# Kernel optimization log

Measured on AMD Instinct MI355X. Metric: run time of the kernel, lower is better.

## Reference

```python
import jax, jax.numpy as jnp
import numpy as np

N_NODES = 100000
N_EDGES = 1600000


def gcn_conv(x, row, col, norm, W, b, n_nodes):
    # PyG GCNConv: h = x @ W; aggregate normalized messages over (A + I); add bias
    h = x @ W                                   # [N, out]
    msg = h[col] * norm[:, None]                # [E+N, out] gather + scale
    out = jax.ops.segment_sum(msg, row, num_segments=n_nodes)  # scatter-add
    return out + b


def _norm_and_loops(edge_index, n_nodes):
    # add self-loops, compute symmetric normalization coefficients
    row = jnp.concatenate([edge_index[0], jnp.arange(n_nodes, dtype=edge_index.dtype)])
    col = jnp.concatenate([edge_index[1], jnp.arange(n_nodes, dtype=edge_index.dtype)])
    deg = jax.ops.segment_sum(jnp.ones_like(row, dtype=jnp.float32), row,
                              num_segments=n_nodes)
    dinv = jnp.where(deg > 0, jax.lax.rsqrt(deg), 0.0)
    norm = dinv[row] * dinv[col]
    return row, col, norm


def reference(x, edge_index, W1, b1, W2, b2, W3, b3):
    n_nodes = x.shape[0]
    row, col, norm = _norm_and_loops(edge_index, n_nodes)
    h = jax.nn.relu(gcn_conv(x, row, col, norm, W1, b1, n_nodes))
    h = jax.nn.relu(gcn_conv(h, row, col, norm, W2, b2, n_nodes))
    h = gcn_conv(h, row, col, norm, W3, b3, n_nodes)
    return jax.nn.log_softmax(h, axis=1)


def setup_inputs() -> dict:
    key = jax.random.key(0)
    ks = jax.random.split(key, 5)
    d_in, d_hid, d_out = 128, 128, 16
    x = jax.random.normal(ks[0], (N_NODES, d_in), dtype=jnp.float32)
    edge_index = jax.random.randint(ks[1], (2, N_EDGES), 0, N_NODES, dtype=jnp.int64)
    s1 = 1.0 / np.sqrt(d_in)
    s3 = 1.0 / np.sqrt(d_hid)
    W1 = jax.random.normal(ks[2], (d_in, d_hid), dtype=jnp.float32) * s1
    W2 = jax.random.normal(ks[3], (d_hid, d_hid), dtype=jnp.float32) * s3
    W3 = jax.random.normal(ks[4], (d_hid, d_out), dtype=jnp.float32) * s3
    return {
        "x": x, "edge_index": edge_index,
        "W1": W1, "b1": jnp.zeros((d_hid,), jnp.float32),
        "W2": W2, "b2": jnp.zeros((d_hid,), jnp.float32),
        "W3": W3, "b3": jnp.zeros((d_out,), jnp.float32),
    }
```

## Files before the change

kernel.cpp:

```cpp
#include <hip/hip_runtime.h>

typedef unsigned int u32;
typedef _Float16 f16;
typedef __attribute__((ext_vector_type(8))) _Float16 half8;
typedef __attribute__((ext_vector_type(2))) _Float16 half2_t;
typedef __attribute__((ext_vector_type(4))) float f32x4;

#define D_IN 128
#define D_HID 128
#define D_OUT 16
#define RPB 128
#define MAXBUCK 1024
#define CHUNK 16384
#define PGRAN 4
#define SLACK 2048


__global__ __launch_bounds__(256) void detect_k(const int* __restrict__ ei,
                                                u32* __restrict__ flag, int n) {
    int i = blockIdx.x * 256 + threadIdx.x;
    if (i < n && (i & 1) && ei[i] != 0) atomicOr(flag, 1u);
}

__device__ inline int load_row(const int* ei, u32 f, int e, int E) {
    return f ? ei[e] : ei[2 * e];
}
__device__ inline int load_col(const int* ei, u32 f, int e, int E) {
    return f ? ei[E + e] : ei[2 * E + 2 * e];
}
__device__ inline int clampi(int v, int n) {
    v = v < 0 ? 0 : v;
    return v >= n ? n - 1 : v;
}
__device__ inline u32 al16(u32 v) { return (v + 15u) & ~15u; }

__global__ __launch_bounds__(256) void hist_k(const int* __restrict__ ei,
                                              const u32* __restrict__ flag,
                                              u32* __restrict__ Hmat,
                                              int E, int N, int NBK, int NB) {
    __shared__ u32 lh[MAXBUCK];
    int tid = threadIdx.x;
    for (int i = tid; i < NBK; i += 256) lh[i] = 0;
    __syncthreads();
    u32 f = *flag;
    int base = blockIdx.x * CHUNK;
    int lim = base + CHUNK < E ? base + CHUNK : E;
    for (int e = base + tid; e < lim; e += 256) {
        int r = clampi(load_row(ei, f, e, E), N);
        atomicAdd(&lh[(u32)r >> 7], 1u);
    }
    __syncthreads();
    for (int i = tid; i < NBK; i += 256)
        Hmat[(size_t)i * NB + blockIdx.x] = lh[i];
}

__global__ __launch_bounds__(256) void scan1(const u32* __restrict__ cnt,
                                             u32* __restrict__ excl,
                                             u32* __restrict__ partial, int n) {
    __shared__ u32 sm[256];
    int tid = threadIdx.x;
    int i = blockIdx.x * 256 + tid;
    u32 v = (i < n) ? cnt[i] : 0u;
    sm[tid] = v;
    __syncthreads();
    for (int off = 1; off < 256; off <<= 1) {
        u32 t = (tid >= off) ? sm[tid - off] : 0u;
        __syncthreads();
        sm[tid] += t;
        __syncthreads();
    }
    if (i < n) excl[i] = sm[tid] - v;
    if (tid == 255) partial[blockIdx.x] = sm[255];
}

__global__ __launch_bounds__(512) void scan2(u32* __restrict__ partial, int nb) {
    __shared__ u32 sm[512];
    int tid = threadIdx.x;
    u32 v = (tid < nb) ? partial[tid] : 0u;
    sm[tid] = v;
    __syncthreads();
    for (int off = 1; off < 512; off <<= 1) {
        u32 t = (tid >= off) ? sm[tid - off] : 0u;
        __syncthreads();
        sm[tid] += t;
        __syncthreads();
    }
    if (tid < nb) partial[tid] = sm[tid] - v;
}

__global__ __launch_bounds__(256) void scan3(u32* __restrict__ excl,
                                             const u32* __restrict__ partial,
                                             int n, int E) {
    int i = blockIdx.x * 256 + threadIdx.x;
    if (i < n) excl[i] += partial[blockIdx.x];
    if (i == 0) excl[n] = (u32)E;
}

__global__ __launch_bounds__(256) void scatter_bd(const int* __restrict__ ei,
                                                  const u32* __restrict__ flag,
                                                  const u32* __restrict__ Hbase,
                                                  u32* __restrict__ bdata,
                                                  int E, int N, int NBK, int NB) {
    __shared__ u32 lbase[MAXBUCK];
    int tid = threadIdx.x;
    for (int i = tid; i < NBK; i += 256)
        lbase[i] = Hbase[(size_t)i * NB + blockIdx.x];
    __syncthreads();
    u32 f = *flag;
    int base = blockIdx.x * CHUNK;
    int lim = base + CHUNK < E ? base + CHUNK : E;
    for (int e = base + tid; e < lim; e += 256) {
        int r = clampi(load_row(ei, f, e, E), N);
        int c = clampi(load_col(ei, f, e, E), N);
        u32 pos = atomicAdd(&lbase[(u32)r >> 7], 1u);
        if (pos < (u32)E) bdata[pos] = ((u32)(r & (RPB - 1)) << 20) | (u32)c;
    }
}

__global__ __launch_bounds__(256) void finalize_k(const u32* __restrict__ bdata,
                                                  const u32* __restrict__ Hbase,
                                                  u32* __restrict__ row_start,
                                                  u32* __restrict__ rend,
                                                  float* __restrict__ dinv,
                                                  u32* __restrict__ ecol,
                                                  int N, int E, int NB) {
    __shared__ u32 smc[RPB];
    __shared__ u32 cur[RPB];
    int b = blockIdx.x;
    int tid = threadIdx.x;
    u32 s = Hbase[(size_t)b * NB];
    u32 t = Hbase[(size_t)(b + 1) * NB];
    u32 pbase = al16(s) + (u32)b * SLACK;
    if (tid < RPB) smc[tid] = 0;
    __syncthreads();
    for (u32 i = s + tid; i < t; i += 256)
        atomicAdd(&smc[bdata[i] >> 20], 1u);
    __syncthreads();
    u32 deg = (tid < RPB) ? smc[tid] : 0;
    u32 pdeg = (deg + PGRAN - 1) & ~(u32)(PGRAN - 1);
    if (tid < RPB) smc[tid] = pdeg;
    __syncthreads();
    for (int off = 1; off < RPB; off <<= 1) {
        u32 tv = (tid < RPB && tid >= off) ? smc[tid - off] : 0u;
        __syncthreads();
        if (tid < RPB) smc[tid] += tv;
        __syncthreads();
    }
    u32 pexcl = (tid < RPB) ? (smc[tid] - pdeg) : 0;
    if (tid < RPB) {
        int r = b * RPB + tid;
        if (r < N) {
            row_start[r] = pbase + pexcl;
            rend[r] = pbase + pexcl + pdeg;
            dinv[r] = rsqrtf((float)(deg + 1u));
        }
        cur[tid] = pbase + pexcl;
    }
    __syncthreads();
    for (u32 i = s + tid; i < t; i += 256) {
        u32 rec = bdata[i];
        u32 pos = atomicAdd(&cur[rec >> 20], 1u);
        ecol[pos] = rec & 0xFFFFFu;
    }
    __syncthreads();
    if (tid < RPB) {
        u32 st = pbase + pexcl;
        for (u32 k = deg; k < pdeg; k++) ecol[st + k] = (u32)N;
    }
}

__global__ __launch_bounds__(256) void reformat_all(const float* __restrict__ W1,
                                                    const float* __restrict__ W2,
                                                    const float* __restrict__ W3,
                                                    f16* __restrict__ W1h, f16* __restrict__ W1l,
                                                    f16* __restrict__ W2h, f16* __restrict__ W2l,
                                                    f16* __restrict__ W3h, f16* __restrict__ W3l,
                                                    f16* __restrict__ hzero,
                                                    f16* __restrict__ h3zero) {
    if (blockIdx.x == 17) {
        int tix = threadIdx.x;
        if (tix < 128) hzero[tix] = (f16)0;
        else if (tix < 144) h3zero[tix - 128] = (f16)0;
        return;
    }
    const float* W;
    f16 *Wh, *Wl;
    int ntiles, bidx;
    if (blockIdx.x < 8) { W = W1; Wh = W1h; Wl = W1l; ntiles = 8; bidx = blockIdx.x; }
    else if (blockIdx.x < 16) { W = W2; Wh = W2h; Wl = W2l; ntiles = 8; bidx = blockIdx.x - 8; }
    else { W = W3; Wh = W3h; Wl = W3l; ntiles = 1; bidx = 0; }
    int idx = bidx * 256 + threadIdx.x;
    int total = 4 * ntiles * 64;
    if (idx >= total) return;
    int lane = idx & 63;
    int st = idx >> 6;
    int t = st % ntiles;
    int s = st / ntiles;
    int Nc = ntiles * 16;
    int n = t * 16 + (lane & 15);
    int kb = lane >> 4;
    half8 vh, vl;
#pragma unroll
    for (int j = 0; j < 8; j++) {
        float w = W[(size_t)(s * 32 + kb * 8 + j) * Nc + n];
        f16 hi = (f16)w;
        f16 lo = (f16)(w - (float)hi);
        vh[j] = hi;
        vl[j] = lo;
    }
    *(half8*)(Wh + (size_t)idx * 8) = vh;
    *(half8*)(Wl + (size_t)idx * 8) = vl;
}


__global__ __launch_bounds__(256) void gemm128_l1(const float* __restrict__ A,
                                                  const f16* __restrict__ Wh,
                                                  const f16* __restrict__ Wl,
                                                  const float* __restrict__ dinv,
                                                  f16* __restrict__ H, int M) {
    int wave = threadIdx.x >> 6, lane = threadIdx.x & 63;
    int mbase = blockIdx.x * 64 + wave * 16;
    int mload = mbase + (lane & 15);
    if (mload >= M) mload = M - 1;
    int kq = lane >> 4;
    f32x4 acc[8];
#pragma unroll
    for (int t = 0; t < 8; t++) acc[t] = (f32x4){0.f, 0.f, 0.f, 0.f};
#pragma unroll
    for (int s = 0; s < 4; s++) {
        const float* ap = A + (size_t)mload * 128 + s * 32 + kq * 8;
        half8 ah, al;
#pragma unroll
        for (int j = 0; j < 8; j++) {
            float v = ap[j];
            f16 hi = (f16)v;
            ah[j] = hi;
            al[j] = (f16)(v - (float)hi);
        }
#pragma unroll
        for (int t = 0; t < 8; t++) {
            half8 bh = *(const half8*)(Wh + (size_t)((s * 8 + t) * 64 + lane) * 8);
            half8 bl = *(const half8*)(Wl + (size_t)((s * 8 + t) * 64 + lane) * 8);
            acc[t] = __builtin_amdgcn_mfma_f32_16x16x32_f16(ah, bh, acc[t], 0, 0, 0);
            acc[t] = __builtin_amdgcn_mfma_f32_16x16x32_f16(ah, bl, acc[t], 0, 0, 0);
            acc[t] = __builtin_amdgcn_mfma_f32_16x16x32_f16(al, bh, acc[t], 0, 0, 0);
        }
    }
    int coln = lane & 15;
    int rbase = mbase + ((lane >> 4) << 2);
    float dsc[4];
#pragma unroll
    for (int i = 0; i < 4; i++) {
        int rr = rbase + i;
        dsc[i] = dinv[rr < M ? rr : M - 1];
    }
#pragma unroll
    for (int t = 0; t < 8; t++) {
#pragma unroll
        for (int i = 0; i < 4; i++) {
            int rr = rbase + i;
            if (rr < M) H[(size_t)rr * 128 + t * 16 + coln] = (f16)(acc[t][i] * dsc[i]);
        }
    }
}

__global__ __launch_bounds__(256) void gemm128_l2(const f16* __restrict__ A,
                                                  const f16* __restrict__ Wh,
                                                  const f16* __restrict__ Wl,
                                                  f16* __restrict__ H, int M) {
    int wave = threadIdx.x >> 6, lane = threadIdx.x & 63;
    int mbase = blockIdx.x * 64 + wave * 16;
    int mload = mbase + (lane & 15);
    if (mload >= M) mload = M - 1;
    int kq = lane >> 4;
    f32x4 acc[8];
#pragma unroll
    for (int t = 0; t < 8; t++) acc[t] = (f32x4){0.f, 0.f, 0.f, 0.f};
#pragma unroll
    for (int s = 0; s < 4; s++) {
        half8 a = *(const half8*)(A + (size_t)mload * 128 + s * 32 + kq * 8);
#pragma unroll
        for (int t = 0; t < 8; t++) {
            half8 bh = *(const half8*)(Wh + (size_t)((s * 8 + t) * 64 + lane) * 8);
            half8 bl = *(const half8*)(Wl + (size_t)((s * 8 + t) * 64 + lane) * 8);
            acc[t] = __builtin_amdgcn_mfma_f32_16x16x32_f16(a, bh, acc[t], 0, 0, 0);
            acc[t] = __builtin_amdgcn_mfma_f32_16x16x32_f16(a, bl, acc[t], 0, 0, 0);
        }
    }
    int coln = lane & 15;
    int rbase = mbase + ((lane >> 4) << 2);
#pragma unroll
    for (int t = 0; t < 8; t++) {
#pragma unroll
        for (int i = 0; i < 4; i++) {
            int rr = rbase + i;
            if (rr < M) H[(size_t)rr * 128 + t * 16 + coln] = (f16)acc[t][i];
        }
    }
}

__global__ __launch_bounds__(256) void gemm16(const f16* __restrict__ A,
                                              const f16* __restrict__ Wh,
                                              const f16* __restrict__ Wl,
                                              f16* __restrict__ H, int M) {
    int wave = threadIdx.x >> 6, lane = threadIdx.x & 63;
    int mbase = blockIdx.x * 64 + wave * 16;
    int mload = mbase + (lane & 15);
    if (mload >= M) mload = M - 1;
    int kq = lane >> 4;
    f32x4 acc = (f32x4){0.f, 0.f, 0.f, 0.f};
#pragma unroll
    for (int s = 0; s < 4; s++) {
        half8 a = *(const half8*)(A + (size_t)mload * 128 + s * 32 + kq * 8);
        half8 bh = *(const half8*)(Wh + (size_t)(s * 64 + lane) * 8);
        half8 bl = *(const half8*)(Wl + (size_t)(s * 64 + lane) * 8);
        acc = __builtin_amdgcn_mfma_f32_16x16x32_f16(a, bh, acc, 0, 0, 0);
        acc = __builtin_amdgcn_mfma_f32_16x16x32_f16(a, bl, acc, 0, 0, 0);
    }
    int coln = lane & 15;
    int rbase = mbase + ((lane >> 4) << 2);
#pragma unroll
    for (int i = 0; i < 4; i++) {
        int rr = rbase + i;
        if (rr < M) H[(size_t)rr * 16 + coln] = (f16)acc[i];
    }
}

__global__ __launch_bounds__(256) void agg128(const f16* __restrict__ h,
                                              const u32* __restrict__ ecol,
                                              const u32* __restrict__ row_start,
                                              const u32* __restrict__ rend,
                                              const float* __restrict__ dinv,
                                              const float* __restrict__ bias,
                                              f16* __restrict__ out, int M) {
    int lane = threadIdx.x & 63;
    int wave = __builtin_amdgcn_readfirstlane(threadIdx.x >> 6);
    int r = blockIdx.x * 4 + wave;
    if (r >= M) return;
    u32 beg = (u32)__builtin_amdgcn_readfirstlane((int)row_start[r]);
    u32 end = (u32)__builtin_amdgcn_readfirstlane((int)rend[r]);
    float dr = dinv[r];
    const char* hb = (const char*)h;
    u32 loff = (u32)lane << 2;
    float ax0 = 0, ay0 = 0, ax1 = 0, ay1 = 0, ax2 = 0, ay2 = 0, ax3 = 0, ay3 = 0;
    u32 e = beg;
    for (; e + 16 <= end; e += 16) {
        const u32* ep = ecol + e;
        u32 c[16];
#pragma unroll
        for (int j = 0; j < 16; j++) c[j] = ep[j];
        half2_t v[16];
#pragma unroll
        for (int j = 0; j < 16; j++)
            v[j] = *(const half2_t*)(hb + ((c[j] << 8) + loff));
#pragma unroll
        for (int j = 0; j < 16; j += 4) {
            ax0 = fmaf((float)v[j][0],     dr, ax0); ay0 = fmaf((float)v[j][1],     dr, ay0);
            ax1 = fmaf((float)v[j + 1][0], dr, ax1); ay1 = fmaf((float)v[j + 1][1], dr, ay1);
            ax2 = fmaf((float)v[j + 2][0], dr, ax2); ay2 = fmaf((float)v[j + 2][1], dr, ay2);
            ax3 = fmaf((float)v[j + 3][0], dr, ax3); ay3 = fmaf((float)v[j + 3][1], dr, ay3);
        }
    }
    for (; e < end; e += 4) {
        const u32* ep = ecol + e;
        u32 c0 = ep[0], c1 = ep[1], c2 = ep[2], c3 = ep[3];
        half2_t v0 = *(const half2_t*)(hb + ((c0 << 8) + loff));
        half2_t v1 = *(const half2_t*)(hb + ((c1 << 8) + loff));
        half2_t v2 = *(const half2_t*)(hb + ((c2 << 8) + loff));
        half2_t v3 = *(const half2_t*)(hb + ((c3 << 8) + loff));
        ax0 = fmaf((float)v0[0], dr, ax0); ay0 = fmaf((float)v0[1], dr, ay0);
        ax1 = fmaf((float)v1[0], dr, ax1); ay1 = fmaf((float)v1[1], dr, ay1);
        ax2 = fmaf((float)v2[0], dr, ax2); ay2 = fmaf((float)v2[1], dr, ay2);
        ax3 = fmaf((float)v3[0], dr, ax3); ay3 = fmaf((float)v3[1], dr, ay3);
    }
    half2_t vs = *(const half2_t*)(hb + (((u32)r << 8) + loff));
    float2 bb = ((const float2*)bias)[lane];
    float ax = ((ax0 + ax1) + (ax2 + ax3)) + fmaf((float)vs[0], dr, bb.x);
    float ay = ((ay0 + ay1) + (ay2 + ay3)) + fmaf((float)vs[1], dr, bb.y);
    ax = fmaxf(ax, 0.f) * dr;
    ay = fmaxf(ay, 0.f) * dr;
    half2_t o;
    o[0] = (f16)ax;
    o[1] = (f16)ay;
    ((half2_t*)out)[(size_t)r * 64 + lane] = o;
}

__global__ __launch_bounds__(256) void agg16_lsm(const f16* __restrict__ h3,
                                                 const u32* __restrict__ ecol,
                                                 const u32* __restrict__ row_start,
                                                 const u32* __restrict__ rend,
                                                 const float* __restrict__ dinv,
                                                 const float* __restrict__ bias,
                                                 float* __restrict__ out, int M) {
    int g = threadIdx.x >> 4, l = threadIdx.x & 15;
    int r = blockIdx.x * 16 + g;
    if (r >= M) return;
    u32 beg = row_start[r], end = rend[r];
    float a0 = 0.f, a1 = 0.f, a2 = 0.f, a3 = 0.f;
    u32 e = beg;
    for (; e + 8 <= end; e += 8) {
        u32 c[8];
#pragma unroll
        for (int j = 0; j < 8; j++) c[j] = ecol[e + j];
        f16 v[8];
#pragma unroll
        for (int j = 0; j < 8; j++) v[j] = h3[(size_t)c[j] * 16 + l];
        a0 += (float)v[0] + (float)v[4];
        a1 += (float)v[1] + (float)v[5];
        a2 += (float)v[2] + (float)v[6];
        a3 += (float)v[3] + (float)v[7];
    }
    if (e < end) {
        u32 c[4];
#pragma unroll
        for (int j = 0; j < 4; j++) c[j] = ecol[e + j];
        f16 v[4];
#pragma unroll
        for (int j = 0; j < 4; j++) v[j] = h3[(size_t)c[j] * 16 + l];
        a0 += (float)v[0];
        a1 += (float)v[1];
        a2 += (float)v[2];
        a3 += (float)v[3];
    }
    float dr = dinv[r];
    float acc = (((a0 + a1) + (a2 + a3)) + (float)h3[(size_t)r * 16 + l]) * dr +
                bias[l];
    float m = acc;
#pragma unroll
    for (int o = 8; o >= 1; o >>= 1) m = fmaxf(m, __shfl_xor(m, o, 16));
    float ex = expf(acc - m);
    float s = ex;
#pragma unroll
    for (int o = 8; o >= 1; o >>= 1) s += __shfl_xor(s, o, 16);
    out[(size_t)r * 16 + l] = acc - m - logf(s);
}


extern "C" void kernel_launch(void* const* d_in, const int* in_sizes, int n_in,
                              void* d_out, int out_size, void* d_ws, size_t ws_size,
                              hipStream_t stream) {
    const float* x = (const float*)d_in[0];
    const int* ei = (const int*)d_in[1];
    const float* W1 = (const float*)d_in[2];
    const float* b1 = (const float*)d_in[3];
    const float* W2 = (const float*)d_in[4];
    const float* b2 = (const float*)d_in[5];
    const float* W3 = (const float*)d_in[6];
    const float* b3 = (const float*)d_in[7];
    int N = in_sizes[0] / D_IN;
    int E = in_sizes[1] / 2;

    int NBK = (N + RPB - 1) / RPB;
    int NB = (E + CHUNK - 1) / CHUNK;
    int L = NBK * NB;
    size_t Epad = ((size_t)E + 16) + (size_t)NBK * SLACK + 256;

    char* p = (char*)d_ws;
    auto alloc = [&](size_t bytes) -> void* {
        void* q = (void*)p;
        p += (bytes + 255) & ~(size_t)255;
        return q;
    };
    u32* flag = (u32*)alloc(256);
    float* dinv = (float*)alloc((size_t)N * 4);
    u32* row_start = (u32*)alloc((size_t)(N + 1) * 4);
    u32* rend = (u32*)alloc((size_t)N * 4);
    u32* partial2 = (u32*)alloc(4096);
    u32* Hmat = (u32*)alloc((size_t)(L + 1) * 4);
    u32* ecol = (u32*)alloc(Epad * 4);
    u32* bdata = (u32*)alloc((size_t)E * 4);
    f16* wf1h = (f16*)alloc(16384 * 2);
    f16* wf1l = (f16*)alloc(16384 * 2);
    f16* wf2h = (f16*)alloc(16384 * 2);
    f16* wf2l = (f16*)alloc(16384 * 2);
    f16* wf3h = (f16*)alloc(2048 * 2);
    f16* wf3l = (f16*)alloc(2048 * 2);
    f16* h = (f16*)alloc((size_t)(N + 1) * 128 * 2);
    f16* act = (f16*)alloc((size_t)N * 128 * 2);
    f16* h3 = (f16*)alloc((size_t)(N + 1) * 16 * 2);
    (void)ws_size; (void)n_in; (void)out_size;

    hipMemsetAsync(flag, 0, 4, stream);

    int nb2 = (L + 255) / 256;

    detect_k<<<32, 256, 0, stream>>>(ei, flag, 8192);
    hist_k<<<NB, 256, 0, stream>>>(ei, flag, Hmat, E, N, NBK, NB);
    scan1<<<nb2, 256, 0, stream>>>(Hmat, Hmat, partial2, L);
    scan2<<<1, 512, 0, stream>>>(partial2, nb2);
    scan3<<<nb2, 256, 0, stream>>>(Hmat, partial2, L, E);
    scatter_bd<<<NB, 256, 0, stream>>>(ei, flag, Hmat, bdata, E, N, NBK, NB);
    finalize_k<<<NBK, 256, 0, stream>>>(bdata, Hmat, row_start, rend, dinv,
                                        ecol, N, E, NB);

    reformat_all<<<18, 256, 0, stream>>>(W1, W2, W3, wf1h, wf1l, wf2h, wf2l,
                                         wf3h, wf3l,
                                         h + (size_t)N * 128,
                                         h3 + (size_t)N * 16);

    int gb = (N + 63) / 64;
    int ab = (N + 3) / 4;
    gemm128_l1<<<gb, 256, 0, stream>>>(x, wf1h, wf1l, dinv, h, N);
    agg128<<<ab, 256, 0, stream>>>(h, ecol, row_start, rend, dinv, b1, act, N);
    gemm128_l2<<<gb, 256, 0, stream>>>(act, wf2h, wf2l, h, N);
    agg128<<<ab, 256, 0, stream>>>(h, ecol, row_start, rend, dinv, b2, act, N);
    gemm16<<<gb, 256, 0, stream>>>(act, wf3h, wf3l, h3, N);
    agg16_lsm<<<(N + 15) / 16, 256, 0, stream>>>(h3, ecol, row_start, rend,
                                                 dinv, b3, (float*)d_out, N);
}
```

Measured before the change: 383.3 us.

## Process two rows per wave in agg128 with interleaved software-pipelined gathers

Each wave in agg128 now aggregates two destination rows, interleaving their 16-edge gather batches and prefetching the next batch before accumulating the current one. This raises memory-level parallelism and hides gather latency. Out-of-range lanes in the final batch are pointed at the sentinel row instead of running a separate tail loop. Row start and end are packed into one uint2 descriptor so each row needs a single load, and agg16_lsm hoists its scalar loads ahead of the loop. The cost is higher register pressure from two 16-entry value arrays, half as many waves in flight, and possible load imbalance when the two paired rows have very different degrees.

After: 381.0 us. About the same (-0.6%).

```diff
diff --git a/kernel.cpp b/kernel.cpp
--- a/kernel.cpp
+++ b/kernel.cpp
@@ -119,8 +119,7 @@
 
 __global__ __launch_bounds__(256) void finalize_k(const u32* __restrict__ bdata,
                                                   const u32* __restrict__ Hbase,
-                                                  u32* __restrict__ row_start,
-                                                  u32* __restrict__ rend,
+                                                  uint2* __restrict__ rdesc,
                                                   float* __restrict__ dinv,
                                                   u32* __restrict__ ecol,
                                                   int N, int E, int NB) {
@@ -150,8 +149,7 @@
     if (tid < RPB) {
         int r = b * RPB + tid;
         if (r < N) {
-            row_start[r] = pbase + pexcl;
-            rend[r] = pbase + pexcl + pdeg;
+            rdesc[r] = make_uint2(pbase + pexcl, pbase + pexcl + pdeg);
             dinv[r] = rsqrtf((float)(deg + 1u));
         }
         cur[tid] = pbase + pexcl;
@@ -328,74 +326,104 @@
 
 __global__ __launch_bounds__(256) void agg128(const f16* __restrict__ h,
                                               const u32* __restrict__ ecol,
-                                              const u32* __restrict__ row_start,
-                                              const u32* __restrict__ rend,
+                                              const uint2* __restrict__ rdesc,
                                               const float* __restrict__ dinv,
                                               const float* __restrict__ bias,
                                               f16* __restrict__ out, int M) {
     int lane = threadIdx.x & 63;
     int wave = __builtin_amdgcn_readfirstlane(threadIdx.x >> 6);
-    int r = blockIdx.x * 4 + wave;
-    if (r >= M) return;
-    u32 beg = (u32)__builtin_amdgcn_readfirstlane((int)row_start[r]);
-    u32 end = (u32)__builtin_amdgcn_readfirstlane((int)rend[r]);
-    float dr = dinv[r];
+    int r0 = (blockIdx.x * 4 + wave) * 2;
+    if (r0 >= M) return;
+    int r1 = (r0 + 1 < M) ? r0 + 1 : r0;
+    uint2 dA = rdesc[r0];
+    uint2 dB = rdesc[r1];
+    u32 eA = (u32)__builtin_amdgcn_readfirstlane((int)dA.x);
+    u32 endA = (u32)__builtin_amdgcn_readfirstlane((int)dA.y);
+    u32 eB = (u32)__builtin_amdgcn_readfirstlane((int)dB.x);
+    u32 endB = (u32)__builtin_amdgcn_readfirstlane((int)dB.y);
+    float drA = dinv[r0], drB = dinv[r1];
     const char* hb = (const char*)h;
     u32 loff = (u32)lane << 2;
-    float ax0 = 0, ay0 = 0, ax1 = 0, ay1 = 0, ax2 = 0, ay2 = 0, ax3 = 0, ay3 = 0;
-    u32 e = beg;
-    for (; e + 16 <= end; e += 16) {
-        const u32* ep = ecol + e;
-        u32 c[16];
-#pragma unroll
-        for (int j = 0; j < 16; j++) c[j] = ep[j];
-        half2_t v[16];
-#pragma unroll
-        for (int j = 0; j < 16; j++)
-            v[j] = *(const half2_t*)(hb + ((c[j] << 8) + loff));
-#pragma unroll
-        for (int j = 0; j < 16; j += 4) {
-            ax0 = fmaf((float)v[j][0],     dr, ax0); ay0 = fmaf((float)v[j][1],     dr, ay0);
-            ax1 = fmaf((float)v[j + 1][0], dr, ax1); ay1 = fmaf((float)v[j + 1][1], dr, ay1);
-            ax2 = fmaf((float)v[j + 2][0], dr, ax2); ay2 = fmaf((float)v[j + 2][1], dr, ay2);
-            ax3 = fmaf((float)v[j + 3][0], dr, ax3); ay3 = fmaf((float)v[j + 3][1], dr, ay3);
-        }
-    }
-    for (; e < end; e += 4) {
-        const u32* ep = ecol + e;
-        u32 c0 = ep[0], c1 = ep[1], c2 = ep[2], c3 = ep[3];
-        half2_t v0 = *(const half2_t*)(hb + ((c0 << 8) + loff));
-        half2_t v1 = *(const half2_t*)(hb + ((c1 << 8) + loff));
-        half2_t v2 = *(const half2_t*)(hb + ((c2 << 8) + loff));
-        half2_t v3 = *(const half2_t*)(hb + ((c3 << 8) + loff));
-        ax0 = fmaf((float)v0[0], dr, ax0); ay0 = fmaf((float)v0[1], dr, ay0);
-        ax1 = fmaf((float)v1[0], dr, ax1); ay1 = fmaf((float)v1[1], dr, ay1);
-        ax2 = fmaf((float)v2[0], dr, ax2); ay2 = fmaf((float)v2[1], dr, ay2);
-        ax3 = fmaf((float)v3[0], dr, ax3); ay3 = fmaf((float)v3[1], dr, ay3);
-    }
-    half2_t vs = *(const half2_t*)(hb + (((u32)r << 8) + loff));
+    u32 sentoff = ((u32)M << 8) + loff;
     float2 bb = ((const float2*)bias)[lane];
-    float ax = ((ax0 + ax1) + (ax2 + ax3)) + fmaf((float)vs[0], dr, bb.x);
-    float ay = ((ay0 + ay1) + (ay2 + ay3)) + fmaf((float)vs[1], dr, bb.y);
-    ax = fmaxf(ax, 0.f) * dr;
-    ay = fmaxf(ay, 0.f) * dr;
-    half2_t o;
-    o[0] = (f16)ax;
-    o[1] = (f16)ay;
-    ((half2_t*)out)[(size_t)r * 64 + lane] = o;
+    half2_t vsA = *(const half2_t*)(hb + (((u32)r0 << 8) + loff));
+    half2_t vsB = *(const half2_t*)(hb + (((u32)r1 << 8) + loff));
+
+#define GATHER16(vv, ebase, endv)                                         \
+    {                                                                     \
+        const u32* ep = ecol + (ebase);                                   \
+        _Pragma("unroll") for (int j = 0; j < 16; j++) {                  \
+            u32 off = (ep[j] << 8) + loff;                                \
+            off = ((ebase) + (u32)j < (endv)) ? off : sentoff;            \
+            vv[j] = *(const half2_t*)(hb + off);                          \
+        }                                                                 \
+    }
+
+    float axA0 = 0, ayA0 = 0, axA1 = 0, ayA1 = 0, axA2 = 0, ayA2 = 0, axA3 = 0, ayA3 = 0;
+    float axB0 = 0, ayB0 = 0, axB1 = 0, ayB1 = 0, axB2 = 0, ayB2 = 0, axB3 = 0, ayB3 = 0;
+    half2_t vA[16], vB[16];
+    GATHER16(vA, eA, endA);
+    GATHER16(vB, eB, endB);
+    bool liveA = true, liveB = true;
+    while (liveA || liveB) {
+        if (liveA) {
+#pragma unroll
+            for (int j = 0; j < 16; j += 4) {
+                axA0 = fmaf((float)vA[j][0],     drA, axA0); ayA0 = fmaf((float)vA[j][1],     drA, ayA0);
+                axA1 = fmaf((float)vA[j + 1][0], drA, axA1); ayA1 = fmaf((float)vA[j + 1][1], drA, ayA1);
+                axA2 = fmaf((float)vA[j + 2][0], drA, axA2); ayA2 = fmaf((float)vA[j + 2][1], drA, ayA2);
+                axA3 = fmaf((float)vA[j + 3][0], drA, axA3); ayA3 = fmaf((float)vA[j + 3][1], drA, ayA3);
+            }
+            eA += 16;
+            liveA = eA < endA;
+            if (liveA) GATHER16(vA, eA, endA);
+        }
+        if (liveB) {
+#pragma unroll
+            for (int j = 0; j < 16; j += 4) {
+                axB0 = fmaf((float)vB[j][0],     drB, axB0); ayB0 = fmaf((float)vB[j][1],     drB, ayB0);
+                axB1 = fmaf((float)vB[j + 1][0], drB, axB1); ayB1 = fmaf((float)vB[j + 1][1], drB, ayB1);
+                axB2 = fmaf((float)vB[j + 2][0], drB, axB2); ayB2 = fmaf((float)vB[j + 2][1], drB, ayB2);
+                axB3 = fmaf((float)vB[j + 3][0], drB, axB3); ayB3 = fmaf((float)vB[j + 3][1], drB, ayB3);
+            }
+            eB += 16;
+            liveB = eB < endB;
+            if (liveB) GATHER16(vB, eB, endB);
+        }
+    }
+#undef GATHER16
+    float ax = ((axA0 + axA1) + (axA2 + axA3)) + fmaf((float)vsA[0], drA, bb.x);
+    float ay = ((ayA0 + ayA1) + (ayA2 + ayA3)) + fmaf((float)vsA[1], drA, bb.y);
+    ax = fmaxf(ax, 0.f) * drA;
+    ay = fmaxf(ay, 0.f) * drA;
+    half2_t oA;
+    oA[0] = (f16)ax;
+    oA[1] = (f16)ay;
+    ((half2_t*)out)[(size_t)r0 * 64 + lane] = oA;
+    float bx = ((axB0 + axB1) + (axB2 + axB3)) + fmaf((float)vsB[0], drB, bb.x);
+    float by = ((ayB0 + ayB1) + (ayB2 + ayB3)) + fmaf((float)vsB[1], drB, bb.y);
+    bx = fmaxf(bx, 0.f) * drB;
+    by = fmaxf(by, 0.f) * drB;
+    half2_t oB;
+    oB[0] = (f16)bx;
+    oB[1] = (f16)by;
+    ((half2_t*)out)[(size_t)r1 * 64 + lane] = oB;
 }
 
 __global__ __launch_bounds__(256) void agg16_lsm(const f16* __restrict__ h3,
                                                  const u32* __restrict__ ecol,
-                                                 const u32* __restrict__ row_start,
-                                                 const u32* __restrict__ rend,
+                                                 const uint2* __restrict__ rdesc,
                                                  const float* __restrict__ dinv,
                                                  const float* __restrict__ bias,
                                                  float* __restrict__ out, int M) {
     int g = threadIdx.x >> 4, l = threadIdx.x & 15;
     int r = blockIdx.x * 16 + g;
     if (r >= M) return;
-    u32 beg = row_start[r], end = rend[r];
+    uint2 d = rdesc[r];
+    u32 beg = d.x, end = d.y;
+    float dr = dinv[r];
+    float bl = bias[l];
+    float self = (float)h3[(size_t)r * 16 + l];
     float a0 = 0.f, a1 = 0.f, a2 = 0.f, a3 = 0.f;
     u32 e = beg;
     for (; e + 8 <= end; e += 8) {
@@ -422,9 +450,7 @@
         a2 += (float)v[2];
         a3 += (float)v[3];
     }
-    float dr = dinv[r];
-    float acc = (((a0 + a1) + (a2 + a3)) + (float)h3[(size_t)r * 16 + l]) * dr +
-                bias[l];
+    float acc = (((a0 + a1) + (a2 + a3)) + self) * dr + bl;
     float m = acc;
 #pragma unroll
     for (int o = 8; o >= 1; o >>= 1) m = fmaxf(m, __shfl_xor(m, o, 16));
@@ -463,8 +489,7 @@
     };
     u32* flag = (u32*)alloc(256);
     float* dinv = (float*)alloc((size_t)N * 4);
-    u32* row_start = (u32*)alloc((size_t)(N + 1) * 4);
-    u32* rend = (u32*)alloc((size_t)N * 4);
+    uint2* rdesc = (uint2*)alloc((size_t)(N + 1) * 8);
     u32* partial2 = (u32*)alloc(4096);
     u32* Hmat = (u32*)alloc((size_t)(L + 1) * 4);
     u32* ecol = (u32*)alloc(Epad * 4);
@@ -490,8 +515,7 @@
     scan2<<<1, 512, 0, stream>>>(partial2, nb2);
     scan3<<<nb2, 256, 0, stream>>>(Hmat, partial2, L, E);
     scatter_bd<<<NB, 256, 0, stream>>>(ei, flag, Hmat, bdata, E, N, NBK, NB);
-    finalize_k<<<NBK, 256, 0, stream>>>(bdata, Hmat, row_start, rend, dinv,
-                                        ecol, N, E, NB);
+    finalize_k<<<NBK, 256, 0, stream>>>(bdata, Hmat, rdesc, dinv, ecol, N, E, NB);
 
     reformat_all<<<18, 256, 0, stream>>>(W1, W2, W3, wf1h, wf1l, wf2h, wf2l,
                                          wf3h, wf3l,
@@ -499,12 +523,12 @@
                                          h3 + (size_t)N * 16);
 
     int gb = (N + 63) / 64;
-    int ab = (N + 3) / 4;
+    int ab = (N + 7) / 8;
     gemm128_l1<<<gb, 256, 0, stream>>>(x, wf1h, wf1l, dinv, h, N);
-    agg128<<<ab, 256, 0, stream>>>(h, ecol, row_start, rend, dinv, b1, act, N);
+    agg128<<<ab, 256, 0, stream>>>(h, ecol, rdesc, dinv, b1, act, N);
     gemm128_l2<<<gb, 256, 0, stream>>>(act, wf2h, wf2l, h, N);
-    agg128<<<ab, 256, 0, stream>>>(h, ecol, row_start, rend, dinv, b2, act, N);
+    agg128<<<ab, 256, 0, stream>>>(h, ecol, rdesc, dinv, b2, act, N);
     gemm16<<<gb, 256, 0, stream>>>(act, wf3h, wf3l, h3, N);
-    agg16_lsm<<<(N + 15) / 16, 256, 0, stream>>>(h3, ecol, row_start, rend,
+    agg16_lsm<<<(N + 15) / 16, 256, 0, stream>>>(h3, ecol, rdesc,
                                                  dinv, b3, (float*)d_out, N);
 }
```
